# Performance work log

Hardware: AMD Instinct MI355X
Metric: run time of the kernel (lower is better)

The kernel has to match this reference:

```python
import jax, jax.numpy as jnp
import numpy as np

B, D_MODEL, D_SAE, K = 8192, 768, 16384, 64


def setup_inputs() -> dict:
    key = jax.random.key(0)
    k1, k2, k3 = jax.random.split(key, 3)
    return {
        "x": jax.random.normal(k1, (B, D_MODEL), dtype=jnp.float32),
        "W_enc": jax.random.normal(k2, (D_MODEL, D_SAE), dtype=jnp.float32) * 0.02,
        "b_enc": jnp.zeros((D_SAE,), dtype=jnp.float32),
        "W_dec": jax.random.normal(k3, (D_SAE, D_MODEL), dtype=jnp.float32) * 0.02,
        "b_dec": jnp.zeros((D_MODEL,), dtype=jnp.float32),
        "k": K,
    }


def reference(x, W_enc, b_enc, W_dec, b_dec, k):
    # encode: [B, d_sae]
    pre_relu = jax.nn.relu(x @ W_enc + b_enc)
    if k >= pre_relu.shape[-1]:
        z = pre_relu
    else:
        topk_vals, topk_idx = jax.lax.top_k(pre_relu, k)  # [B, k]
        z = jnp.zeros_like(pre_relu)
        z = jnp.take_along_axis(
            jnp.zeros_like(pre_relu), topk_idx, axis=-1
        )  # placeholder not needed; use scatter via at[]
        rows = jnp.arange(pre_relu.shape[0])[:, None]  # [B, 1]
        z = jnp.zeros_like(pre_relu).at[rows, topk_idx].set(topk_vals)
    recon = z @ W_dec + b_dec
    return (z, recon)
```

## Files before the change

### kernel.cpp

```cpp
#include <hip/hip_runtime.h>
#include <cstdint>

#define NROWS 8192
#define DM    768
#define DS    16384

typedef __attribute__((ext_vector_type(8))) short          bf16x8;
typedef __attribute__((ext_vector_type(8))) unsigned short u16x8;
typedef __attribute__((ext_vector_type(4))) float          f32x4;

__device__ __forceinline__ unsigned short f2bf(float f) {
  unsigned u = __float_as_uint(f);
  unsigned r = u + 0x7fffu + ((u >> 16) & 1u);
  return (unsigned short)(r >> 16);
}


__global__ __launch_bounds__(256) void cvt_x_bf16(const float* __restrict__ x,
                                                  unsigned short* __restrict__ xb) {
  int i = blockIdx.x * 256 + threadIdx.x;
  float4 v = ((const float4*)x)[i];
  ushort4 o;
  o.x = f2bf(v.x); o.y = f2bf(v.y); o.z = f2bf(v.z); o.w = f2bf(v.w);
  ((ushort4*)xb)[i] = o;
}

__global__ __launch_bounds__(256) void transpose_w(const float* __restrict__ We,
                                                   float* __restrict__ WTf,
                                                   unsigned short* __restrict__ WTb) {
  __shared__ float t[32][33];
  const int c0 = blockIdx.x * 32;
  const int r0 = blockIdx.y * 32;
  const int tx = threadIdx.x & 31, ty = threadIdx.x >> 5;
#pragma unroll
  for (int i = 0; i < 4; ++i)
    t[ty + i * 8][tx] = We[(size_t)(r0 + ty + i * 8) * DS + c0 + tx];
  __syncthreads();
#pragma unroll
  for (int i = 0; i < 4; ++i) {
    float v = t[tx][ty + i * 8];
    size_t o = (size_t)(c0 + ty + i * 8) * DM + r0 + tx;
    WTf[o] = v;
    WTb[o] = f2bf(v);
  }
}

__global__ __launch_bounds__(256) void sae_encode_bf16(
    const unsigned short* __restrict__ xb,
    const unsigned short* __restrict__ WTb,
    const float* __restrict__ be,
    float* __restrict__ pre)
{
  __shared__ __align__(16) short As[128 * 64];
  __shared__ __align__(16) short Bs[128 * 64];

  const int tid  = threadIdx.x;
  const int lane = tid & 63;
  const int w    = tid >> 6;
  const int wm   = w >> 1, wn = w & 1;
  const int m0   = blockIdx.y * 128, n0 = blockIdx.x * 128;
  const int l15  = lane & 15, q = lane >> 4, l7 = lane & 7;

  f32x4 acc[4][4];
  const f32x4 zero4 = {0.f, 0.f, 0.f, 0.f};
#pragma unroll
  for (int i = 0; i < 4; ++i)
#pragma unroll
    for (int j = 0; j < 4; ++j) acc[i][j] = zero4;

  for (int k0 = 0; k0 < DM; k0 += 64) {
#pragma unroll
    for (int i = 0; i < 4; ++i) {
      int idx = tid + i * 256;
      int m = idx >> 3, g = idx & 7;
      int ldsb = m * 128 + (((g ^ (m & 7))) << 4);
      u16x8 va = *(const u16x8*)(xb  + (size_t)(m0 + m) * DM + k0 + g * 8);
      *(u16x8*)((char*)As + ldsb) = va;
      u16x8 vb = *(const u16x8*)(WTb + (size_t)(n0 + m) * DM + k0 + g * 8);
      *(u16x8*)((char*)Bs + ldsb) = vb;
    }
    __syncthreads();

#pragma unroll
    for (int h = 0; h < 2; ++h) {
      const int gsw = (((h * 4 + q) ^ l7) << 4);
      bf16x8 af[4], bfr[4];
#pragma unroll
      for (int t = 0; t < 4; ++t) {
        af[t]  = *(const bf16x8*)((const char*)As + (wm * 64 + t * 16 + l15) * 128 + gsw);
        bfr[t] = *(const bf16x8*)((const char*)Bs + (wn * 64 + t * 16 + l15) * 128 + gsw);
      }
#pragma unroll
      for (int mf = 0; mf < 4; ++mf)
#pragma unroll
        for (int nf = 0; nf < 4; ++nf)
          acc[mf][nf] = __builtin_amdgcn_mfma_f32_16x16x32_bf16(
              af[mf], bfr[nf], acc[mf][nf], 0, 0, 0);
    }
    __syncthreads();
  }

#pragma unroll
  for (int nf = 0; nf < 4; ++nf) {
    const int gcol = n0 + wn * 64 + nf * 16 + l15;
    const float bias = be[gcol];
#pragma unroll
    for (int mf = 0; mf < 4; ++mf) {
#pragma unroll
      for (int r = 0; r < 4; ++r) {
        int grow = m0 + wm * 64 + mf * 16 + q * 4 + r;
        pre[(size_t)grow * DS + gcol] = acc[mf][nf][r] + bias;
      }
    }
  }
}

#define MARGIN 1.2e-2f
#define FINE_LO 0x3C800000u
#define FINE_HI 0x40800000u
#define HICAP 256
#define BDCAP 512
#define SELCAP 160

__global__ __launch_bounds__(256) void sae_topk_fused(
    float* __restrict__ z,
    float* __restrict__ recon,
    const float* __restrict__ x,
    const float* __restrict__ WTf,
    const float* __restrict__ be,
    const float* __restrict__ Wd,
    const float* __restrict__ bd,
    const int* __restrict__ kptr)
{
  const int row = blockIdx.x;
  const int tid = threadIdx.x;
  int k = *kptr; if (k < 1) k = 1; if (k > 128) k = 128;

  float* zrow = z + (size_t)row * DS;

  __shared__ int   fine[2048];
  __shared__ int   part[256];
  __shared__ int   s_above, s_pos;
  __shared__ uint2 sh_LU;
  __shared__ float xs[DM];
  __shared__ int   hi_idx[HICAP];
  __shared__ float hi_val[HICAP];
  __shared__ int   bd_idx[BDCAP];
  __shared__ float cex[BDCAP];
  __shared__ int   s_nh, s_nb;
  __shared__ int   sidx[SELCAP];
  __shared__ float sval[SELCAP];

#pragma unroll
  for (int i = 0; i < 8; ++i) fine[tid + i * 256] = 0;
  if (tid == 0) { s_above = 0; s_pos = 0; s_nh = 0; s_nb = 0; }
  for (int i = tid; i < DM; i += 256) xs[i] = x[(size_t)row * DM + i];
  __syncthreads();

  int above_c = 0, pos_c = 0;
  {
    const float4* src = (const float4*)zrow;
#pragma unroll
    for (int jj = 0; jj < 16; ++jj) {
      float4 v = src[tid + jj * 256];
      float c4[4] = {v.x, v.y, v.z, v.w};
#pragma unroll
      for (int c = 0; c < 4; ++c) {
        if (c4[c] > 0.f) {
          ++pos_c;
          unsigned b = __float_as_uint(c4[c]);
          if (b >= FINE_HI) ++above_c;
          else if (b >= FINE_LO) atomicAdd(&fine[(b >> 15) - (FINE_LO >> 15)], 1);
        }
      }
    }
  }
  if (above_c) atomicAdd(&s_above, above_c);
  if (pos_c)   atomicAdd(&s_pos, pos_c);
  __syncthreads();

  int p = 0;
#pragma unroll
  for (int i = 0; i < 8; ++i) p += fine[tid * 8 + i];
  part[tid] = p;
  __syncthreads();
  for (int off = 1; off < 256; off <<= 1) {
    int v = part[tid];
    int add = (tid + off < 256) ? part[tid + off] : 0;
    __syncthreads();
    part[tid] = v + add;
    __syncthreads();
  }
  const int tot_fine = part[0];

  if (s_pos < k) {
    if (tid == 0) sh_LU = make_uint2(0u, 0u);
  } else if (s_above >= k) {
    if (tid == 0) sh_LU = make_uint2(FINE_HI, 0x7F7FFFFFu);
  } else if (s_above + tot_fine < k) {
    if (tid == 0) sh_LU = make_uint2(0u, FINE_LO);
  } else {
    int nxt = (tid == 255) ? 0 : part[tid + 1];
    if (s_above + part[tid] >= k && (tid == 255 || s_above + nxt < k)) {
      int acc = s_above + nxt;
      int bin = 0;
      for (int i = 7; i >= 0; --i) {
        acc += fine[tid * 8 + i];
        if (acc >= k) { bin = tid * 8 + i; break; }
      }
      unsigned L = (unsigned)(bin + (int)(FINE_LO >> 15)) << 15;
      sh_LU = make_uint2(L, L + (1u << 15));
    }
  }
  __syncthreads();

  unsigned ulo, uhi;
  {
    const uint2 t2 = sh_LU;
    if (t2.y == 0u) {
      ulo = 0u; uhi = 0u;
    } else {
      float Lf = __uint_as_float(t2.x) - MARGIN;
      ulo = (Lf > 0.f) ? __float_as_uint(Lf) : 0u;
      float Uf = __uint_as_float(t2.y) + MARGIN;
      uhi = __float_as_uint(Uf);
    }
  }

  {
    const float4 z4 = make_float4(0.f, 0.f, 0.f, 0.f);
    float4* p4 = (float4*)zrow;
#pragma unroll
    for (int jj = 0; jj < 16; ++jj) {
      float4 v = p4[tid + jj * 256];
      int base = (tid + jj * 256) * 4;
      float c4[4] = {v.x, v.y, v.z, v.w};
#pragma unroll
      for (int c = 0; c < 4; ++c) {
        if (c4[c] > 0.f) {
          unsigned b = __float_as_uint(c4[c]);
          if (b > uhi) {
            int pp = atomicAdd(&s_nh, 1);
            if (pp < HICAP) { hi_idx[pp] = base + c; hi_val[pp] = c4[c]; }
          } else if (b > ulo) {
            int pp = atomicAdd(&s_nb, 1);
            if (pp < BDCAP) bd_idx[pp] = base + c;
          }
        }
      }
      p4[tid + jj * 256] = z4;
    }
  }
  __syncthreads();
  const int nh = (s_nh < HICAP) ? s_nh : HICAP;
  const int nb = (s_nb < BDCAP) ? s_nb : BDCAP;

  for (int c = tid; c < nb; c += 256) {
    const float* wcol = WTf + (size_t)bd_idx[c] * DM;
    float s = 0.f;
#pragma unroll 8
    for (int i = 0; i < DM; ++i) s = fmaf(xs[i], wcol[i], s);
    cex[c] = s + be[bd_idx[c]];
  }
  __syncthreads();

  int nh_kept, need;
  if (nh <= k) {
    nh_kept = nh;
    need = k - nh;
    for (int t = tid; t < nh; t += 256) {
      int myi = hi_idx[t];
      int r = 0;
      for (int c = 0; c < nh; ++c) r += (hi_idx[c] < myi);
      sidx[r] = myi; sval[r] = hi_val[t];
    }
  } else {
    nh_kept = k;
    need = 0;
    for (int t = tid; t < nh; t += 256) {
      float er = hi_val[t];
      int myi = hi_idx[t];
      int r = 0;
      for (int c = 0; c < nh; ++c)
        r += (hi_val[c] > er) || (hi_val[c] == er && hi_idx[c] < myi);
      if (r < k) { sidx[r] = myi; sval[r] = er; }
    }
  }
  __syncthreads();

  for (int t = tid; t < nb; t += 256) {
    float er = fmaxf(cex[t], 0.f);
    int myi = bd_idx[t];
    int r = 0;
    for (int c = 0; c < nb; ++c) {
      float ec = fmaxf(cex[c], 0.f);
      r += (ec > er) || (ec == er && bd_idx[c] < myi);
    }
    if (r < need) { sidx[nh_kept + r] = myi; sval[nh_kept + r] = er; }
  }
  __syncthreads();

  const int nsel = nh_kept + (need < nb ? need : nb);

  if (tid < nsel) zrow[sidx[tid]] = sval[tid];

  float a0 = bd[tid], a1 = bd[tid + 256], a2 = bd[tid + 512];
  for (int r = 0; r < nsel; ++r) {
    float v = sval[r];
    const float* wr = Wd + (size_t)sidx[r] * DM;
    a0 = fmaf(v, wr[tid],       a0);
    a1 = fmaf(v, wr[tid + 256], a1);
    a2 = fmaf(v, wr[tid + 512], a2);
  }
  float* rr = recon + (size_t)row * DM;
  rr[tid] = a0; rr[tid + 256] = a1; rr[tid + 512] = a2;
}

#define BM 128
#define BN 128
#define BK 32

__global__ __launch_bounds__(256) void sae_encode_gemm(
    const float* __restrict__ x, const float* __restrict__ We,
    const float* __restrict__ be, float* __restrict__ pre)
{
  __shared__ float As2[BK][BM];
  __shared__ float Bs2[BK][BN];

  const int tid = threadIdx.x;
  const int bx  = blockIdx.x;
  const int by  = blockIdx.y;
  const int c0  = (tid & 15) * 4;
  const int r0  = (tid >> 4) * 4;

  float acc[2][2][4][4];
#pragma unroll
  for (int p = 0; p < 2; ++p)
#pragma unroll
    for (int qq = 0; qq < 2; ++qq)
#pragma unroll
      for (int i = 0; i < 4; ++i)
#pragma unroll
        for (int j = 0; j < 4; ++j) acc[p][qq][i][j] = 0.f;

  const float* xblk = x  + (size_t)by * BM * DM;
  const float* wblk = We + (size_t)bx * BN;

  for (int k0 = 0; k0 < DM; k0 += BK) {
#pragma unroll
    for (int i = 0; i < 4; ++i) {
      int s  = tid + i * 256;
      int m  = s >> 3;
      int kk4 = (s & 7) << 2;
      float4 v = *(const float4*)(xblk + (size_t)m * DM + (k0 + kk4));
      int cs = m ^ kk4;
      As2[kk4 + 0][cs] = v.x;
      As2[kk4 + 1][cs] = v.y;
      As2[kk4 + 2][cs] = v.z;
      As2[kk4 + 3][cs] = v.w;
    }
#pragma unroll
    for (int i = 0; i < 4; ++i) {
      int s  = tid + i * 256;
      int kk = s >> 5;
      int n  = (s & 31) << 2;
      *(float4*)&Bs2[kk][n] = *(const float4*)(wblk + (size_t)(k0 + kk) * DS + n);
    }
    __syncthreads();
#pragma unroll 4
    for (int kk = 0; kk < BK; ++kk) {
      const int kkm = kk & 0x1C;
      const int ra  = r0 ^ kkm;
      float4 a0 = *(const float4*)&As2[kk][ra];
      float4 a1 = *(const float4*)&As2[kk][ra + 64];
      float4 b0 = *(const float4*)&Bs2[kk][c0];
      float4 b1 = *(const float4*)&Bs2[kk][c0 + 64];
      float av[2][4] = {{a0.x, a0.y, a0.z, a0.w}, {a1.x, a1.y, a1.z, a1.w}};
      float bv[2][4] = {{b0.x, b0.y, b0.z, b0.w}, {b1.x, b1.y, b1.z, b1.w}};
#pragma unroll
      for (int p = 0; p < 2; ++p)
#pragma unroll
        for (int qq = 0; qq < 2; ++qq)
#pragma unroll
          for (int i = 0; i < 4; ++i)
#pragma unroll
            for (int j = 0; j < 4; ++j)
              acc[p][qq][i][j] = fmaf(av[p][i], bv[qq][j], acc[p][qq][i][j]);
    }
    __syncthreads();
  }

  const int row0 = by * BM + r0;
  const int col0 = bx * BN + c0;
  float bias[2][4];
#pragma unroll
  for (int qq = 0; qq < 2; ++qq)
#pragma unroll
    for (int j = 0; j < 4; ++j) bias[qq][j] = be[col0 + qq * 64 + j];
#pragma unroll
  for (int p = 0; p < 2; ++p)
#pragma unroll
    for (int i = 0; i < 4; ++i) {
      float* dst = pre + (size_t)(row0 + p * 64 + i) * DS + col0;
#pragma unroll
      for (int qq = 0; qq < 2; ++qq) {
        float4 o;
        o.x = fmaxf(acc[p][qq][i][0] + bias[qq][0], 0.f);
        o.y = fmaxf(acc[p][qq][i][1] + bias[qq][1], 0.f);
        o.z = fmaxf(acc[p][qq][i][2] + bias[qq][2], 0.f);
        o.w = fmaxf(acc[p][qq][i][3] + bias[qq][3], 0.f);
        *(float4*)(dst + qq * 64) = o;
      }
    }
}

__global__ __launch_bounds__(256) void sae_topk_decode(
    float* __restrict__ z, float* __restrict__ recon,
    const float* __restrict__ Wd, const float* __restrict__ bd,
    const int* __restrict__ kptr)
{
  const int row = blockIdx.x;
  const int tid = threadIdx.x;
  int k = *kptr;
  if (k < 1) k = 1;
  if (k > 1024) k = 1024;

  float* zrow = z + (size_t)row * DS;

  unsigned u[64];
  {
    const float4* src = (const float4*)zrow;
#pragma unroll
    for (int jj = 0; jj < 16; ++jj) {
      float4 v = src[tid + jj * 256];
      u[jj * 4 + 0] = (v.x > 0.f) ? __float_as_uint(v.x) : 0u;
      u[jj * 4 + 1] = (v.y > 0.f) ? __float_as_uint(v.y) : 0u;
      u[jj * 4 + 2] = (v.z > 0.f) ? __float_as_uint(v.z) : 0u;
      u[jj * 4 + 3] = (v.w > 0.f) ? __float_as_uint(v.w) : 0u;
    }
  }

  __shared__ int red[8];
  unsigned tbits = 0;
  for (int bit = 30; bit >= 0; --bit) {
    unsigned cand = tbits | (1u << bit);
    int c = 0;
#pragma unroll
    for (int j = 0; j < 64; ++j) c += (u[j] >= cand);
#pragma unroll
    for (int off = 32; off > 0; off >>= 1) c += __shfl_down(c, off, 64);
    if ((tid & 63) == 0) red[tid >> 6] = c;
    __syncthreads();
    int tot = red[0] + red[1] + red[2] + red[3];
    __syncthreads();
    if (tot >= k) tbits = cand;
  }

  int cnt_gt = 0, cnt_eq = 0;
  if (tbits != 0) {
    int c1 = 0, c2 = 0;
#pragma unroll
    for (int j = 0; j < 64; ++j) { c1 += (u[j] > tbits); c2 += (u[j] == tbits); }
#pragma unroll
    for (int off = 32; off > 0; off >>= 1) {
      c1 += __shfl_down(c1, off, 64);
      c2 += __shfl_down(c2, off, 64);
    }
    if ((tid & 63) == 0) { red[tid >> 6] = c1; red[4 + (tid >> 6)] = c2; }
    __syncthreads();
    cnt_gt = red[0] + red[1] + red[2] + red[3];
    cnt_eq = red[4] + red[5] + red[6] + red[7];
    __syncthreads();
  }
  const int needed = k - cnt_gt;

  __shared__ int eq_n;
  __shared__ int eq_keep;
  __shared__ int eq_idx[256];
  const bool rare = (tbits != 0) && (cnt_eq > needed);
  if (rare) {
    if (tid == 0) eq_n = 0;
    __syncthreads();
#pragma unroll
    for (int jj = 0; jj < 16; ++jj)
#pragma unroll
      for (int c = 0; c < 4; ++c) {
        int j = jj * 4 + c;
        if (u[j] == tbits) {
          int p = atomicAdd(&eq_n, 1);
          if (p < 256) eq_idx[p] = (tid + jj * 256) * 4 + c;
        }
      }
    __syncthreads();
    if (tid == 0) {
      int n = eq_n < 256 ? eq_n : 256;
      for (int a = 1; a < n; ++a) {
        int key = eq_idx[a]; int b = a - 1;
        while (b >= 0 && eq_idx[b] > key) { eq_idx[b + 1] = eq_idx[b]; --b; }
        eq_idx[b + 1] = key;
      }
      int kp = needed < n ? needed : n;
      eq_keep = kp < 0 ? 0 : kp;
    }
    __syncthreads();
  }

  unsigned long long mask = 0ull;
#pragma unroll
  for (int jj = 0; jj < 16; ++jj)
#pragma unroll
    for (int c = 0; c < 4; ++c) {
      int j = jj * 4 + c;
      bool s;
      if (tbits == 0) {
        s = (u[j] > 0u);
      } else if (u[j] > tbits) {
        s = true;
      } else if (u[j] == tbits) {
        if (!rare) s = true;
        else {
          int idx = (tid + jj * 256) * 4 + c;
          s = false;
          for (int e = 0; e < eq_keep; ++e)
            if (eq_idx[e] == idx) { s = true; break; }
        }
      } else s = false;
      if (s) mask |= (1ull << j);
    }
  const int mycount = __popcll(mask);

  __shared__ int scan[256];
  scan[tid] = mycount;
  __syncthreads();
  for (int off = 1; off < 256; off <<= 1) {
    int v = scan[tid];
    int add = (tid >= off) ? scan[tid - off] : 0;
    __syncthreads();
    scan[tid] = v + add;
    __syncthreads();
  }
  const int total = scan[255];
  int pos = scan[tid] - mycount;

  __shared__ float s_val[1024];
  __shared__ int   s_idx[1024];
  {
    float4* dst = (float4*)zrow;
#pragma unroll
    for (int jj = 0; jj < 16; ++jj) {
      float4 wv;
      float* wp = (float*)&wv;
#pragma unroll
      for (int c = 0; c < 4; ++c) {
        int j = jj * 4 + c;
        bool s = (mask >> j) & 1ull;
        float val = __uint_as_float(u[j]);
        wp[c] = s ? val : 0.f;
        if (s && pos < 1024) {
          s_idx[pos] = (tid + jj * 256) * 4 + c;
          s_val[pos] = val;
          ++pos;
        }
      }
      dst[tid + jj * 256] = wv;
    }
  }
  __syncthreads();

  float a0 = bd[tid], a1 = bd[tid + 256], a2 = bd[tid + 512];
  const int n = total < 1024 ? total : 1024;
#pragma unroll 4
  for (int i = 0; i < n; ++i) {
    float v = s_val[i];
    const float* wr = Wd + (size_t)s_idx[i] * DM;
    a0 = fmaf(v, wr[tid],       a0);
    a1 = fmaf(v, wr[tid + 256], a1);
    a2 = fmaf(v, wr[tid + 512], a2);
  }
  float* rr = recon + (size_t)row * DM;
  rr[tid] = a0; rr[tid + 256] = a1; rr[tid + 512] = a2;
}

extern "C" void kernel_launch(void* const* d_in, const int* in_sizes, int n_in,
                              void* d_out, int out_size, void* d_ws, size_t ws_size,
                              hipStream_t stream) {
  (void)in_sizes; (void)n_in; (void)out_size;

  const float* x     = (const float*)d_in[0];
  const float* W_enc = (const float*)d_in[1];
  const float* b_enc = (const float*)d_in[2];
  const float* W_dec = (const float*)d_in[3];
  const float* b_dec = (const float*)d_in[4];
  const int*   kp    = (const int*)d_in[5];

  float* z     = (float*)d_out;
  float* recon = z + (size_t)NROWS * DS;

  const size_t sz_WTf = (size_t)DS * DM * 4;
  const size_t sz_WTb = (size_t)DS * DM * 2;
  const size_t sz_xb  = (size_t)NROWS * DM * 2;
  const size_t need   = sz_WTf + sz_WTb + sz_xb;

  if (ws_size >= need) {
    float*          WTf = (float*)d_ws;
    unsigned short* WTb = (unsigned short*)((char*)d_ws + sz_WTf);
    unsigned short* xb  = (unsigned short*)((char*)d_ws + sz_WTf + sz_WTb);

    cvt_x_bf16<<<(NROWS * DM) / (4 * 256), 256, 0, stream>>>(x, xb);
    transpose_w<<<dim3(DS / 32, DM / 32), 256, 0, stream>>>(W_enc, WTf, WTb);
    sae_encode_bf16<<<dim3(DS / 128, NROWS / 128), 256, 0, stream>>>(xb, WTb, b_enc, z);
    sae_topk_fused<<<NROWS, 256, 0, stream>>>(z, recon, x, WTf, b_enc, W_dec, b_dec, kp);
  } else {
    sae_encode_gemm<<<dim3(DS / BN, NROWS / BM), 256, 0, stream>>>(x, W_enc, b_enc, z);
    sae_topk_decode<<<NROWS, 256, 0, stream>>>(z, recon, W_dec, b_dec, kp);
  }
}
```

Measured before the change: 0.9997 ms.

## Store encoder pre-activations as bf16 and stage each row in shared memory

The encode GEMM now writes its pre-activations as bf16 into the first half of each z row (stride 32768 shorts), which halves the intermediate write and the top-k read traffic. The top-k kernel reads the bf16 row once, copies it into a 32 KB shared-memory buffer, and runs the second classification pass from LDS instead of re-reading global memory. Zeroing of z becomes a separate pure-store loop. Because the candidate values are now bf16, the selection margin is widened to cover the coarser precision, which admits more borderline candidates for exact fp32 recomputation. The larger LDS footprint may also lower occupancy.

New measurement: 1.110 ms. 11.0% more time.

```diff
diff --git a/kernel.cpp b/kernel.cpp
--- a/kernel.cpp
+++ b/kernel.cpp
@@ -4,6 +4,7 @@
 #define NROWS 8192
 #define DM    768
 #define DS    16384
+#define PREB_STRIDE 32768
 
 typedef __attribute__((ext_vector_type(8))) short          bf16x8;
 typedef __attribute__((ext_vector_type(8))) unsigned short u16x8;
@@ -49,7 +50,7 @@
     const unsigned short* __restrict__ xb,
     const unsigned short* __restrict__ WTb,
     const float* __restrict__ be,
-    float* __restrict__ pre)
+    unsigned short* __restrict__ preb)
 {
   __shared__ __align__(16) short As[128 * 64];
   __shared__ __align__(16) short Bs[128 * 64];
@@ -109,13 +110,13 @@
 #pragma unroll
       for (int r = 0; r < 4; ++r) {
         int grow = m0 + wm * 64 + mf * 16 + q * 4 + r;
-        pre[(size_t)grow * DS + gcol] = acc[mf][nf][r] + bias;
-      }
-    }
-  }
-}
-
-#define MARGIN 1.2e-2f
+        preb[(size_t)grow * PREB_STRIDE + gcol] = f2bf(acc[mf][nf][r] + bias);
+      }
+    }
+  }
+}
+
+#define MARGIN 0.04f
 #define FINE_LO 0x3C800000u
 #define FINE_HI 0x40800000u
 #define HICAP 256
@@ -137,7 +138,9 @@
   int k = *kptr; if (k < 1) k = 1; if (k > 128) k = 128;
 
   float* zrow = z + (size_t)row * DS;
-
+  const unsigned short* zrowb = (const unsigned short*)zrow;
+
+  __shared__ __align__(16) unsigned short rowb[DS];
   __shared__ int   fine[2048];
   __shared__ int   part[256];
   __shared__ int   s_above, s_pos;
@@ -159,16 +162,18 @@
 
   int above_c = 0, pos_c = 0;
   {
-    const float4* src = (const float4*)zrow;
-#pragma unroll
-    for (int jj = 0; jj < 16; ++jj) {
-      float4 v = src[tid + jj * 256];
-      float c4[4] = {v.x, v.y, v.z, v.w};
-#pragma unroll
-      for (int c = 0; c < 4; ++c) {
-        if (c4[c] > 0.f) {
+    const u16x8* srcb = (const u16x8*)zrowb;
+#pragma unroll
+    for (int it = 0; it < 8; ++it) {
+      int idx = tid + it * 256;
+      u16x8 v = srcb[idx];
+      *(u16x8*)&rowb[idx * 8] = v;
+#pragma unroll
+      for (int e = 0; e < 8; ++e) {
+        unsigned short us = (unsigned short)v[e];
+        if (us > 0 && us < 0x8000) {
           ++pos_c;
-          unsigned b = __float_as_uint(c4[c]);
+          unsigned b = ((unsigned)us) << 16;
           if (b >= FINE_HI) ++above_c;
           else if (b >= FINE_LO) atomicAdd(&fine[(b >> 15) - (FINE_LO >> 15)], 1);
         }
@@ -228,28 +233,31 @@
   }
 
   {
+#pragma unroll
+    for (int it = 0; it < 8; ++it) {
+      int idx = tid + it * 256;
+      u16x8 v = *(const u16x8*)&rowb[idx * 8];
+#pragma unroll
+      for (int e = 0; e < 8; ++e) {
+        unsigned short us = (unsigned short)v[e];
+        if (us > 0 && us < 0x8000) {
+          unsigned b = ((unsigned)us) << 16;
+          if (b > uhi) {
+            int pp = atomicAdd(&s_nh, 1);
+            if (pp < HICAP) { hi_idx[pp] = idx * 8 + e; hi_val[pp] = __uint_as_float(b); }
+          } else if (b > ulo) {
+            int pp = atomicAdd(&s_nb, 1);
+            if (pp < BDCAP) bd_idx[pp] = idx * 8 + e;
+          }
+        }
+      }
+    }
+  }
+  {
     const float4 z4 = make_float4(0.f, 0.f, 0.f, 0.f);
     float4* p4 = (float4*)zrow;
 #pragma unroll
-    for (int jj = 0; jj < 16; ++jj) {
-      float4 v = p4[tid + jj * 256];
-      int base = (tid + jj * 256) * 4;
-      float c4[4] = {v.x, v.y, v.z, v.w};
-#pragma unroll
-      for (int c = 0; c < 4; ++c) {
-        if (c4[c] > 0.f) {
-          unsigned b = __float_as_uint(c4[c]);
-          if (b > uhi) {
-            int pp = atomicAdd(&s_nh, 1);
-            if (pp < HICAP) { hi_idx[pp] = base + c; hi_val[pp] = c4[c]; }
-          } else if (b > ulo) {
-            int pp = atomicAdd(&s_nb, 1);
-            if (pp < BDCAP) bd_idx[pp] = base + c;
-          }
-        }
-      }
-      p4[tid + jj * 256] = z4;
-    }
+    for (int jj = 0; jj < 16; ++jj) p4[tid + jj * 256] = z4;
   }
   __syncthreads();
   const int nh = (s_nh < HICAP) ? s_nh : HICAP;
@@ -608,7 +616,8 @@
 
     cvt_x_bf16<<<(NROWS * DM) / (4 * 256), 256, 0, stream>>>(x, xb);
     transpose_w<<<dim3(DS / 32, DM / 32), 256, 0, stream>>>(W_enc, WTf, WTb);
-    sae_encode_bf16<<<dim3(DS / 128, NROWS / 128), 256, 0, stream>>>(xb, WTb, b_enc, z);
+    sae_encode_bf16<<<dim3(DS / 128, NROWS / 128), 256, 0, stream>>>(
+        xb, WTb, b_enc, (unsigned short*)z);
     sae_topk_fused<<<NROWS, 256, 0, stream>>>(z, recon, x, WTf, b_enc, W_dec, b_dec, kp);
   } else {
     sae_encode_gemm<<<dim3(DS / BN, NROWS / BM), 256, 0, stream>>>(x, W_enc, b_enc, z);
```
